# Kernel tuning notes

Measured on AMD Instinct MI355X. Metric: run time of the kernel, lower is better.

## Reference

```python
import jax, jax.numpy as jnp
import numpy as np

ALPHA = 0.25
GAMMA = 2.0
IMG = 512.0


def _focal(t, logits):
    # faithful to get_focal_loss: sigmoid -> alpha/focal weighting -> BCE -> mean
    c = jax.nn.sigmoid(logits)
    alpha_factor = jnp.where(t == 1.0, ALPHA, 1.0 - ALPHA)
    focal_weight = alpha_factor * jnp.where(t == 1.0, 1.0 - c, c) ** GAMMA
    bce = -(t * jnp.log(c) + (1.0 - t) * jnp.log(1.0 - c))
    return (focal_weight * bce).mean()


def setup_inputs() -> dict:
    key = jax.random.key(0)
    kc, kr, kd, ka1, ka2, kb1, kb2, kl = jax.random.split(key, 8)
    B, A, C = 32, 200000, 10000
    classifications = jax.random.normal(kc, (B, C), dtype=jnp.float32)
    regressions = 0.1 * jax.random.normal(kr, (B, A, 4), dtype=jnp.float32)
    box_dist = jax.random.normal(kd, (B, A), dtype=jnp.float32)
    # anchors: random boxes inside a 512x512 image
    ctr = jax.random.uniform(ka1, (A, 2), minval=0.0, maxval=IMG)
    wh = jax.random.uniform(ka2, (A, 2), minval=16.0, maxval=256.0)
    anchor = jnp.concatenate([ctr - 0.5 * wh, ctr + 0.5 * wh], axis=1)
    anchors = anchor[None].astype(jnp.float32)  # [1, A, 4]
    # annotations: [B, 1, 7] = one gt box + 3 noun class indices (stored as float)
    gctr = jax.random.uniform(kb1, (B, 1, 2), minval=128.0, maxval=384.0)
    gwh = jax.random.uniform(kb2, (B, 1, 2), minval=64.0, maxval=256.0)
    gbox = jnp.concatenate([gctr - 0.5 * gwh, gctr + 0.5 * gwh], axis=2)
    nouns = jax.random.randint(kl, (B, 1, 3), 0, C).astype(jnp.float32)
    annotations = jnp.concatenate([gbox, nouns], axis=2).astype(jnp.float32)
    return {
        "classifications": classifications,
        "regressions": regressions,
        "box_dist": box_dist,
        "anchors": anchors,
        "annotations": annotations,
    }


def reference(classifications, regressions, box_dist, anchors, annotations):
    anchor = anchors[0]                              # [A, 4]
    aw = anchor[:, 2] - anchor[:, 0]
    ah = anchor[:, 3] - anchor[:, 1]
    ax = anchor[:, 0] + 0.5 * aw
    ay = anchor[:, 1] + 0.5 * ah
    area_a = aw * ah
    scale = jnp.array([0.1, 0.1, 0.2, 0.2], dtype=jnp.float32)

    def per_image(cls_j, reg_j, bd_j, ann_j):
        ann = ann_j[0]                               # [7] single annotation
        nouns = ann[4:7].astype(jnp.int32)
        target_nouns = jnp.zeros_like(cls_j).at[nouns].set(1.0)
        cls_loss = _focal(target_nouns, cls_j)
        # IoU of all anchors vs the single gt box; argmax over 1 box == box 0
        b = ann[:4]
        iw = jnp.clip(jnp.minimum(anchor[:, 2], b[2]) - jnp.maximum(anchor[:, 0], b[0]), 0.0)
        ih = jnp.clip(jnp.minimum(anchor[:, 3], b[3]) - jnp.maximum(anchor[:, 1], b[1]), 0.0)
        inter = iw * ih
        ua = jnp.clip(area_a + (b[2] - b[0]) * (b[3] - b[1]) - inter, 1e-8)
        iou_max = inter / ua                          # [A]
        pos = (iou_max >= 0.5).astype(cls_j.dtype)    # [A] float 0/1
        bbox_loss = _focal(pos, bd_j)
        # Faithful to the torch code: positive_indices.long() used as GATHER indices
        pidx = pos.astype(jnp.int32)                  # values in {0,1}
        aw_pi = aw[pidx]; ah_pi = ah[pidx]
        ax_pi = ax[pidx]; ay_pi = ay[pidx]
        # assigned_annotations rows are all identical (single gt, argmax==0),
        # so the 0/1 gather is an identity on the gt box
        gw_raw = b[2] - b[0]
        gh_raw = b[3] - b[1]
        gx = b[0] + 0.5 * gw_raw
        gy = b[1] + 0.5 * gh_raw
        gw = jnp.clip(gw_raw, 1.0)
        gh = jnp.clip(gh_raw, 1.0)
        targets = jnp.stack(
            [(gx - ax_pi) / aw_pi,
             (gy - ay_pi) / ah_pi,
             jnp.log(gw / aw_pi),
             jnp.log(gh / ah_pi)], axis=1) / scale    # [A, 4]
        diff = jnp.abs(targets - reg_j[pidx])
        rl = jnp.where(diff <= 1.0 / 9.0, 0.5 * 9.0 * diff ** 2, diff - 0.5 / 9.0).mean()
        reg_loss = jnp.where(pidx.sum() > 0, rl, jnp.zeros((), rl.dtype))
        return cls_loss, bbox_loss, reg_loss

    cl, bl, rl = jax.vmap(per_image)(classifications, regressions, box_dist, annotations)
    return (cl.mean(keepdims=True), bl.mean(keepdims=True), rl.mean(keepdims=True))
```

## Files before the change

kernel.cpp:

```cpp
#include <hip/hip_runtime.h>

#define B_IMG 32
#define N_A   200000
#define N_C   10000

#define NCH   32
#define CHUNK (N_A / NCH)
#define NCC   4
#define CCHUNK (N_C / NCC)

#define WS_FOCAL 0
#define WS_CNT   (B_IMG * NCH)
#define WS_CLS   (2 * B_IMG * NCH)

__device__ __forceinline__ float focal_elem(float x, bool t) {
    float e = __expf(-x);
    float r = __builtin_amdgcn_rcpf(1.0f + e);
    float L = __logf(1.0f + e);
    if (t) { float om = e * r; return 0.25f * om * om * L; }
    else   { return 0.75f * r * r * (x + L); }
}

__device__ __forceinline__ double wave_red(double v) {
#pragma unroll
    for (int o = 32; o; o >>= 1) v += __shfl_down(v, o, 64);
    return v;
}

__global__ __launch_bounds__(256) void main_kernel(
    const float* __restrict__ cls, const float* __restrict__ bd,
    const float* __restrict__ anc, const float* __restrict__ ann,
    double* __restrict__ ws)
{
    const int tid = threadIdx.x;
    const int lane = tid & 63, wv = tid >> 6;
    __shared__ double sred[2][4];

    if (blockIdx.x < B_IMG * NCH) {
        const int j  = blockIdx.x >> 5;
        const int ch = blockIdx.x & 31;
        const int a0 = ch * CHUNK;

        const float b0 = ann[j*7+0], b1 = ann[j*7+1], b2 = ann[j*7+2], b3 = ann[j*7+3];
        const float barea = (b2 - b0) * (b3 - b1);
        const float* __restrict__ bdr = bd + (size_t)j * N_A;

        float fsum = 0.0f, cnt = 0.0f;
        for (int i = a0 + tid; i < a0 + CHUNK; i += 256) {
            const float4 av = ((const float4*)anc)[i];
            float iw = fmaxf(fminf(av.z, b2) - fmaxf(av.x, b0), 0.0f);
            float ih = fmaxf(fminf(av.w, b3) - fmaxf(av.y, b1), 0.0f);
            float inter = iw * ih;
            float ua = fmaxf((av.z - av.x) * (av.w - av.y) + barea - inter, 1e-8f);
            bool pos = (2.0f * inter >= ua);
            fsum += focal_elem(bdr[i], pos);
            cnt  += pos ? 1.0f : 0.0f;
        }
        double fv = wave_red((double)fsum);
        double cv = wave_red((double)cnt);
        if (lane == 0) { sred[0][wv] = fv; sred[1][wv] = cv; }
        __syncthreads();
        if (tid == 0) {
            ws[WS_FOCAL + j * NCH + ch] = sred[0][0] + sred[0][1] + sred[0][2] + sred[0][3];
            ws[WS_CNT   + j * NCH + ch] = sred[1][0] + sred[1][1] + sred[1][2] + sred[1][3];
        }
    } else {
        const int bb = blockIdx.x - B_IMG * NCH;
        const int j  = bb >> 2;
        const int cc = bb & 3;
        const int c0 = cc * CCHUNK;
        const int n0 = (int)ann[j*7+4], n1 = (int)ann[j*7+5], n2 = (int)ann[j*7+6];
        const float* __restrict__ cj = cls + (size_t)j * N_C;
        float fsum = 0.0f;
        for (int i = c0 + tid; i < c0 + CCHUNK; i += 256) {
            bool t = (i == n0) || (i == n1) || (i == n2);
            fsum += focal_elem(cj[i], t);
        }
        double v = wave_red((double)fsum);
        if (lane == 0) sred[0][wv] = v;
        __syncthreads();
        if (tid == 0)
            ws[WS_CLS + j * NCC + cc] = sred[0][0] + sred[0][1] + sred[0][2] + sred[0][3];
    }
}

__global__ void final_kernel(
    const float* __restrict__ anc, const float* __restrict__ ann,
    const float* __restrict__ reg, const double* __restrict__ ws,
    float* __restrict__ out)
{
    int t = threadIdx.x;
    double cl = 0.0, bl = 0.0, rl = 0.0;
    if (t < B_IMG) {
        int j = t;
        double fsum = 0.0, npos = 0.0, csum = 0.0;
        for (int ch = 0; ch < NCH; ++ch) {
            fsum += ws[WS_FOCAL + j * NCH + ch];
            npos += ws[WS_CNT   + j * NCH + ch];
        }
        for (int cc = 0; cc < NCC; ++cc) csum += ws[WS_CLS + j * NCC + cc];
        cl = csum / (double)N_C;
        bl = fsum / (double)N_A;

        float b0 = ann[j*7+0], b1 = ann[j*7+1], b2 = ann[j*7+2], b3 = ann[j*7+3];
        float gw_raw = b2 - b0, gh_raw = b3 - b1;
        float gx = b0 + 0.5f * gw_raw, gy = b1 + 0.5f * gh_raw;
        float gw = fmaxf(gw_raw, 1.0f), gh = fmaxf(gh_raw, 1.0f);
        double s[2];
#pragma unroll
        for (int p = 0; p < 2; ++p) {
            float x0 = anc[p*4+0], y0 = anc[p*4+1], x1 = anc[p*4+2], y1 = anc[p*4+3];
            float aw = x1 - x0, ah = y1 - y0;
            float ax = x0 + 0.5f * aw, ay = y0 + 0.5f * ah;
            float tg[4];
            tg[0] = ((gx - ax) / aw) / 0.1f;
            tg[1] = ((gy - ay) / ah) / 0.1f;
            tg[2] = logf(gw / aw) / 0.2f;
            tg[3] = logf(gh / ah) / 0.2f;
            const float* rj = reg + (size_t)j * N_A * 4 + p * 4;
            double ssum = 0.0;
#pragma unroll
            for (int k = 0; k < 4; ++k) {
                float d = fabsf(tg[k] - rj[k]);
                float v = (d <= (1.0f / 9.0f)) ? (0.5f * 9.0f * d * d) : (d - 0.5f / 9.0f);
                ssum += (double)v;
            }
            s[p] = ssum;
        }
        double rlv = (((double)N_A - npos) * s[0] + npos * s[1]) / (4.0 * (double)N_A);
        rl = (npos > 0.0) ? rlv : 0.0;
    }
    cl = wave_red(cl);
    bl = wave_red(bl);
    rl = wave_red(rl);
    if (t == 0) {
        out[0] = (float)(cl / B_IMG);
        out[1] = (float)(bl / B_IMG);
        out[2] = (float)(rl / B_IMG);
    }
}

extern "C" void kernel_launch(void* const* d_in, const int* in_sizes, int n_in,
                              void* d_out, int out_size, void* d_ws, size_t ws_size,
                              hipStream_t stream) {
    const float* cls = (const float*)d_in[0];
    const float* reg = (const float*)d_in[1];
    const float* bd  = (const float*)d_in[2];
    const float* anc = (const float*)d_in[3];
    const float* ann = (const float*)d_in[4];
    float* out = (float*)d_out;
    double* ws = (double*)d_ws;

    hipLaunchKernelGGL(main_kernel, dim3(B_IMG * NCH + B_IMG * NCC), dim3(256), 0, stream,
                       cls, bd, anc, ann, ws);
    hipLaunchKernelGGL(final_kernel, dim3(1), dim3(64), 0, stream, anc, ann, reg, ws, out);
}
```

Baseline: 21.55 us.

## Fuse final reduction into main kernel via last-block atomic counter

Merges the final reduction kernel into the main kernel. Each block bumps an atomic counter after writing its partials, and the last block to finish performs the cross-block reduction and writes the outputs. The grid also changes from 32 to 60 anchor chunks per image, with image and chunk indices decoded via a 64-slot layout. This removes the second kernel launch and its dependency gap, but adds a memset of the counter on the stream plus atomic and fence overhead.

```diff
diff --git a/kernel.cpp b/kernel.cpp
--- a/kernel.cpp
+++ b/kernel.cpp
@@ -4,14 +4,19 @@
 #define N_A   200000
 #define N_C   10000
 
-#define NCH   32
-#define CHUNK (N_A / NCH)
-#define NCC   4
+#define NCH    60
+#define CHUNK  3334
+#define NCC    4
 #define CCHUNK (N_C / NCC)
+#define SLOTS  64
+#define GRID   (B_IMG * SLOTS)
 
 #define WS_FOCAL 0
 #define WS_CNT   (B_IMG * NCH)
 #define WS_CLS   (2 * B_IMG * NCH)
+#define WS_CTR_BYTES ((size_t)(2 * B_IMG * NCH + B_IMG * NCC) * 8)
+
+typedef float f4 __attribute__((ext_vector_type(4)));
 
 __device__ __forceinline__ float focal_elem(float x, bool t) {
     float e = __expf(-x);
@@ -27,27 +32,30 @@
     return v;
 }
 
-__global__ __launch_bounds__(256) void main_kernel(
+__global__ __launch_bounds__(256) void fused_kernel(
     const float* __restrict__ cls, const float* __restrict__ bd,
     const float* __restrict__ anc, const float* __restrict__ ann,
-    double* __restrict__ ws)
+    const float* __restrict__ reg, double* __restrict__ ws,
+    unsigned int* __restrict__ ctr, float* __restrict__ out)
 {
     const int tid = threadIdx.x;
     const int lane = tid & 63, wv = tid >> 6;
+    const int j  = blockIdx.x >> 6;
+    const int ch = blockIdx.x & 63;
     __shared__ double sred[2][4];
+    __shared__ int s_last;
+    const f4* __restrict__ anc4 = (const f4*)anc;
 
-    if (blockIdx.x < B_IMG * NCH) {
-        const int j  = blockIdx.x >> 5;
-        const int ch = blockIdx.x & 31;
+    if (ch < NCH) {
         const int a0 = ch * CHUNK;
-
+        const int a1 = min(a0 + CHUNK, N_A);
         const float b0 = ann[j*7+0], b1 = ann[j*7+1], b2 = ann[j*7+2], b3 = ann[j*7+3];
         const float barea = (b2 - b0) * (b3 - b1);
         const float* __restrict__ bdr = bd + (size_t)j * N_A;
 
         float fsum = 0.0f, cnt = 0.0f;
-        for (int i = a0 + tid; i < a0 + CHUNK; i += 256) {
-            const float4 av = ((const float4*)anc)[i];
+        for (int i = a0 + tid; i < a1; i += 256) {
+            const f4 av = anc4[i];
             float iw = fmaxf(fminf(av.z, b2) - fmaxf(av.x, b0), 0.0f);
             float ih = fmaxf(fminf(av.w, b3) - fmaxf(av.y, b1), 0.0f);
             float inter = iw * ih;
@@ -65,9 +73,7 @@
             ws[WS_CNT   + j * NCH + ch] = sred[1][0] + sred[1][1] + sred[1][2] + sred[1][3];
         }
     } else {
-        const int bb = blockIdx.x - B_IMG * NCH;
-        const int j  = bb >> 2;
-        const int cc = bb & 3;
+        const int cc = ch - NCH;
         const int c0 = cc * CCHUNK;
         const int n0 = (int)ann[j*7+4], n1 = (int)ann[j*7+5], n2 = (int)ann[j*7+6];
         const float* __restrict__ cj = cls + (size_t)j * N_C;
@@ -82,27 +88,30 @@
         if (tid == 0)
             ws[WS_CLS + j * NCC + cc] = sred[0][0] + sred[0][1] + sred[0][2] + sred[0][3];
     }
-}
 
-__global__ void final_kernel(
-    const float* __restrict__ anc, const float* __restrict__ ann,
-    const float* __restrict__ reg, const double* __restrict__ ws,
-    float* __restrict__ out)
-{
-    int t = threadIdx.x;
+    if (tid == 0) {
+        __threadfence();
+        unsigned int old = atomicAdd(ctr, 1u);
+        s_last = (old == GRID - 1) ? 1 : 0;
+    }
+    __syncthreads();
+    if (!s_last) return;
+    __threadfence();
+
+    int t = tid;
     double cl = 0.0, bl = 0.0, rl = 0.0;
     if (t < B_IMG) {
-        int j = t;
+        int jj = t;
         double fsum = 0.0, npos = 0.0, csum = 0.0;
-        for (int ch = 0; ch < NCH; ++ch) {
-            fsum += ws[WS_FOCAL + j * NCH + ch];
-            npos += ws[WS_CNT   + j * NCH + ch];
+        for (int c = 0; c < NCH; ++c) {
+            fsum += ws[WS_FOCAL + jj * NCH + c];
+            npos += ws[WS_CNT   + jj * NCH + c];
         }
-        for (int cc = 0; cc < NCC; ++cc) csum += ws[WS_CLS + j * NCC + cc];
+        for (int c = 0; c < NCC; ++c) csum += ws[WS_CLS + jj * NCC + c];
         cl = csum / (double)N_C;
         bl = fsum / (double)N_A;
 
-        float b0 = ann[j*7+0], b1 = ann[j*7+1], b2 = ann[j*7+2], b3 = ann[j*7+3];
+        float b0 = ann[jj*7+0], b1 = ann[jj*7+1], b2 = ann[jj*7+2], b3 = ann[jj*7+3];
         float gw_raw = b2 - b0, gh_raw = b3 - b1;
         float gx = b0 + 0.5f * gw_raw, gy = b1 + 0.5f * gh_raw;
         float gw = fmaxf(gw_raw, 1.0f), gh = fmaxf(gh_raw, 1.0f);
@@ -117,7 +126,7 @@
             tg[1] = ((gy - ay) / ah) / 0.1f;
             tg[2] = logf(gw / aw) / 0.2f;
             tg[3] = logf(gh / ah) / 0.2f;
-            const float* rj = reg + (size_t)j * N_A * 4 + p * 4;
+            const float* rj = reg + (size_t)jj * N_A * 4 + p * 4;
             double ssum = 0.0;
 #pragma unroll
             for (int k = 0; k < 4; ++k) {
@@ -130,13 +139,15 @@
         double rlv = (((double)N_A - npos) * s[0] + npos * s[1]) / (4.0 * (double)N_A);
         rl = (npos > 0.0) ? rlv : 0.0;
     }
-    cl = wave_red(cl);
-    bl = wave_red(bl);
-    rl = wave_red(rl);
-    if (t == 0) {
-        out[0] = (float)(cl / B_IMG);
-        out[1] = (float)(bl / B_IMG);
-        out[2] = (float)(rl / B_IMG);
+    if (tid < 64) {
+        cl = wave_red(cl);
+        bl = wave_red(bl);
+        rl = wave_red(rl);
+        if (tid == 0) {
+            out[0] = (float)(cl / B_IMG);
+            out[1] = (float)(bl / B_IMG);
+            out[2] = (float)(rl / B_IMG);
+        }
     }
 }
 
@@ -150,8 +161,9 @@
     const float* ann = (const float*)d_in[4];
     float* out = (float*)d_out;
     double* ws = (double*)d_ws;
+    unsigned int* ctr = (unsigned int*)((char*)d_ws + WS_CTR_BYTES);
 
-    hipLaunchKernelGGL(main_kernel, dim3(B_IMG * NCH + B_IMG * NCC), dim3(256), 0, stream,
-                       cls, bd, anc, ann, ws);
-    hipLaunchKernelGGL(final_kernel, dim3(1), dim3(64), 0, stream, anc, ann, reg, ws, out);
+    hipMemsetAsync(ctr, 0, sizeof(unsigned int), stream);
+    hipLaunchKernelGGL(fused_kernel, dim3(GRID), dim3(256), 0, stream,
+                       cls, bd, anc, ann, reg, ws, ctr, out);
 }
```

Result: slower. 66.94 us (+210.6%).
